# Kernel tuning notes

Measured on AMD Instinct MI355X. Metric: run time of the kernel, lower is better.

The kernel has to match this reference:

```python
import jax, jax.numpy as jnp
import numpy as np

KERNEL_SIZE = 9

def setup_inputs() -> dict:
    key = jax.random.key(0)
    k1, k2 = jax.random.split(key)
    x = jax.random.normal(k1, (32, 16384, 8), dtype=jnp.float32)
    W = jax.random.normal(k2, (8, KERNEL_SIZE), dtype=jnp.float32) * 0.05  # 'random_normal' init
    b = jnp.zeros((1,), dtype=jnp.float32)
    return {"x": x, "W": W, "b": b}

def reference(x, W, b):
    # x: (B, S, F); W: (F, K); b: (1,)
    K = W.shape[1]
    S = x.shape[1]
    new_steps = S - K  # matches original: steps - kernel_size
    base = x[:, :new_steps, :] * W[:, 0]          # (B, N, F)
    peaks = jnp.zeros_like(base)
    # loop over small fixed kernel (K-1 = 8 iterations), vectorized over B, N, F
    for k in range(K - 1):
        shifted = x[:, k:k + new_steps, :] * W[:, k + 1]  # (B, N, F)
        peaks = peaks + jnp.abs(base - shifted)
    return peaks + b  # bias (1,) broadcasts over features, as in original
```

## Files before the change

### kernel.cpp

```cpp
#include <hip/hip_runtime.h>

#define BATCH  32
#define S_DIM  16384
#define F_DIM  8
#define K_DIM  9
#define N_DIM  (S_DIM - K_DIM)
#define NPB    256
#define CHUNKS 528

__global__ __launch_bounds__(256) void peak2peak_kernel(
    const float* __restrict__ x,
    const float* __restrict__ W,
    const float* __restrict__ bias,
    float* __restrict__ out)
{
    __shared__ float4 lds4[CHUNKS];

    const int t  = threadIdx.x;
    const int b  = blockIdx.y;
    const int n0 = blockIdx.x << 8;

    const float* xbase = x + ((long)b * S_DIM + n0) * F_DIM;
    const int climit = 2 * (S_DIM - n0);

#pragma unroll
    for (int i = 0; i < 3; ++i) {
        int c = t + i * 256;
        if (c < CHUNKS && c < climit) {
            float4 v = *reinterpret_cast<const float4*>(xbase + c * 4);
            *reinterpret_cast<float4*>(
                reinterpret_cast<char*>(lds4) + ((c ^ ((c >> 3) & 7)) << 4)) = v;
        }
    }
    __syncthreads();

    const float bb = bias[0];
    float res[F_DIM];

#pragma unroll
    for (int j = 0; j < 2; ++j) {
        float4 rv[8];
#pragma unroll
        for (int k = 0; k < 8; ++k) {
            int row = t + k;
            int byteoff = ((2 * row + j) ^ ((row >> 2) & 7)) << 4;
            rv[k] = *reinterpret_cast<const float4*>(
                reinterpret_cast<const char*>(lds4) + byteoff);
        }
        float rr0[4] = { rv[0].x, rv[0].y, rv[0].z, rv[0].w };
        float basev[4], acc[4];
#pragma unroll
        for (int f = 0; f < 4; ++f) {
            basev[f] = rr0[f] * W[(4 * j + f) * K_DIM];
            acc[f]   = 0.f;
        }
#pragma unroll
        for (int k = 0; k < 8; ++k) {
            float rr[4] = { rv[k].x, rv[k].y, rv[k].z, rv[k].w };
#pragma unroll
            for (int f = 0; f < 4; ++f) {
                acc[f] += fabsf(basev[f] - rr[f] * W[(4 * j + f) * K_DIM + k + 1]);
            }
        }
#pragma unroll
        for (int f = 0; f < 4; ++f) res[4 * j + f] = acc[f] + bb;
    }

    const int n = n0 + t;
    if (n < N_DIM) {
        float* orow = out + ((long)b * N_DIM + n) * F_DIM;
        float4 o0 = { res[0], res[1], res[2], res[3] };
        float4 o1 = { res[4], res[5], res[6], res[7] };
        *reinterpret_cast<float4*>(orow)     = o0;
        *reinterpret_cast<float4*>(orow + 4) = o1;
    }
}

extern "C" void kernel_launch(void* const* d_in, const int* in_sizes, int n_in,
                              void* d_out, int out_size, void* d_ws, size_t ws_size,
                              hipStream_t stream) {
    const float* x    = (const float*)d_in[0];
    const float* W    = (const float*)d_in[1];
    const float* bias = (const float*)d_in[2];
    float* out        = (float*)d_out;

    dim3 grid(S_DIM / NPB, BATCH);
    peak2peak_kernel<<<grid, 256, 0, stream>>>(x, W, bias, out);
}
```

Measured before the change: 12.62 us.

## Replace LDS staging with per-thread register windows computing four outputs each

Removes the shared-memory staging and barrier. Each thread instead loads an 11-row sliding window directly from global memory into registers and computes four consecutive output rows. Outputs are written with nontemporal stores. This trades LDS traffic and synchronisation for redundant, less coalesced global loads that must be served from cache, and for higher register pressure.

```diff
diff --git a/kernel.cpp b/kernel.cpp
--- a/kernel.cpp
+++ b/kernel.cpp
@@ -5,8 +5,9 @@
 #define F_DIM  8
 #define K_DIM  9
 #define N_DIM  (S_DIM - K_DIM)
-#define NPB    256
-#define CHUNKS 528
+#define R_OUT  4
+
+typedef __attribute__((ext_vector_type(4))) float f32x4;
 
 __global__ __launch_bounds__(256) void peak2peak_kernel(
     const float* __restrict__ x,
@@ -14,65 +15,51 @@
     const float* __restrict__ bias,
     float* __restrict__ out)
 {
-    __shared__ float4 lds4[CHUNKS];
+    const int t = threadIdx.x;
+    const int b = blockIdx.y;
+    const int n = (blockIdx.x * 256 + t) * R_OUT;
+    if (n >= N_DIM) return;
 
-    const int t  = threadIdx.x;
-    const int b  = blockIdx.y;
-    const int n0 = blockIdx.x << 8;
+    const float* xrow = x + ((long)b * S_DIM + n) * F_DIM;
 
-    const float* xbase = x + ((long)b * S_DIM + n0) * F_DIM;
-    const int climit = 2 * (S_DIM - n0);
-
+    f32x4 r[R_OUT + 7][2];
 #pragma unroll
-    for (int i = 0; i < 3; ++i) {
-        int c = t + i * 256;
-        if (c < CHUNKS && c < climit) {
-            float4 v = *reinterpret_cast<const float4*>(xbase + c * 4);
-            *reinterpret_cast<float4*>(
-                reinterpret_cast<char*>(lds4) + ((c ^ ((c >> 3) & 7)) << 4)) = v;
-        }
+    for (int i = 0; i < R_OUT + 7; ++i) {
+        r[i][0] = *reinterpret_cast<const f32x4*>(xrow + i * F_DIM);
+        r[i][1] = *reinterpret_cast<const f32x4*>(xrow + i * F_DIM + 4);
     }
-    __syncthreads();
 
     const float bb = bias[0];
-    float res[F_DIM];
 
+    float res[R_OUT][F_DIM];
 #pragma unroll
-    for (int j = 0; j < 2; ++j) {
-        float4 rv[8];
+    for (int i = 0; i < R_OUT; ++i) {
+        float basev[F_DIM], acc[F_DIM];
 #pragma unroll
-        for (int k = 0; k < 8; ++k) {
-            int row = t + k;
-            int byteoff = ((2 * row + j) ^ ((row >> 2) & 7)) << 4;
-            rv[k] = *reinterpret_cast<const float4*>(
-                reinterpret_cast<const char*>(lds4) + byteoff);
-        }
-        float rr0[4] = { rv[0].x, rv[0].y, rv[0].z, rv[0].w };
-        float basev[4], acc[4];
-#pragma unroll
-        for (int f = 0; f < 4; ++f) {
-            basev[f] = rr0[f] * W[(4 * j + f) * K_DIM];
+        for (int f = 0; f < F_DIM; ++f) {
+            basev[f] = r[i][f >> 2][f & 3] * W[f * K_DIM];
             acc[f]   = 0.f;
         }
 #pragma unroll
-        for (int k = 0; k < 8; ++k) {
-            float rr[4] = { rv[k].x, rv[k].y, rv[k].z, rv[k].w };
+        for (int k = 0; k < K_DIM - 1; ++k) {
 #pragma unroll
-            for (int f = 0; f < 4; ++f) {
-                acc[f] += fabsf(basev[f] - rr[f] * W[(4 * j + f) * K_DIM + k + 1]);
+            for (int f = 0; f < F_DIM; ++f) {
+                acc[f] += fabsf(basev[f] - r[i + k][f >> 2][f & 3] * W[f * K_DIM + k + 1]);
             }
         }
 #pragma unroll
-        for (int f = 0; f < 4; ++f) res[4 * j + f] = acc[f] + bb;
+        for (int f = 0; f < F_DIM; ++f) res[i][f] = acc[f] + bb;
     }
 
-    const int n = n0 + t;
-    if (n < N_DIM) {
-        float* orow = out + ((long)b * N_DIM + n) * F_DIM;
-        float4 o0 = { res[0], res[1], res[2], res[3] };
-        float4 o1 = { res[4], res[5], res[6], res[7] };
-        *reinterpret_cast<float4*>(orow)     = o0;
-        *reinterpret_cast<float4*>(orow + 4) = o1;
+    float* orow = out + ((long)b * N_DIM + n) * F_DIM;
+#pragma unroll
+    for (int i = 0; i < R_OUT; ++i) {
+        if (n + i < N_DIM) {
+            f32x4 o0 = { res[i][0], res[i][1], res[i][2], res[i][3] };
+            f32x4 o1 = { res[i][4], res[i][5], res[i][6], res[i][7] };
+            __builtin_nontemporal_store(o0, reinterpret_cast<f32x4*>(orow + i * F_DIM));
+            __builtin_nontemporal_store(o1, reinterpret_cast<f32x4*>(orow + i * F_DIM + 4));
+        }
     }
 }
 
@@ -84,6 +71,9 @@
     const float* bias = (const float*)d_in[2];
     float* out        = (float*)d_out;
 
-    dim3 grid(S_DIM / NPB, BATCH);
+    const int groups_per_batch = (N_DIM + R_OUT - 1) / R_OUT;
+    const int blocks_per_batch = (groups_per_batch + 255) / 256;
+    dim3 grid(blocks_per_batch, BATCH);
+
     peak2peak_kernel<<<grid, 256, 0, stream>>>(x, W, bias, out);
 }
```

After: 37.93 us. 201% more time.

## Compute four outputs per thread with larger tiles to reuse staged rows

Applied to the files above, without the earlier changes.

Each thread now computes four consecutive output rows instead of one, and each block covers 1024 rows instead of 256. A thread reads 12 LDS vectors per feature half where it used to read 8 per single row, so LDS traffic and the halo overhead per output drop. The subtract is folded into an FMA. In exchange the kernel uses more registers and LDS per block and launches fewer blocks (16×32), which lowers occupancy and parallelism for a memory-bound kernel, and the output stores are now strided per thread.

```diff
diff --git a/kernel.cpp b/kernel.cpp
--- a/kernel.cpp
+++ b/kernel.cpp
@@ -5,8 +5,11 @@
 #define F_DIM  8
 #define K_DIM  9
 #define N_DIM  (S_DIM - K_DIM)
-#define NPB    256
-#define CHUNKS 528
+#define NPB    1024
+#define R_OUT  4
+#define CHUNKS 2064
+
+typedef __attribute__((ext_vector_type(4))) float f32x4;
 
 __global__ __launch_bounds__(256) void peak2peak_kernel(
     const float* __restrict__ x,
@@ -14,65 +17,72 @@
     const float* __restrict__ bias,
     float* __restrict__ out)
 {
-    __shared__ float4 lds4[CHUNKS];
+    __shared__ f32x4 lds4[CHUNKS];
 
     const int t  = threadIdx.x;
     const int b  = blockIdx.y;
-    const int n0 = blockIdx.x << 8;
+    const int n0 = blockIdx.x * NPB;
 
     const float* xbase = x + ((long)b * S_DIM + n0) * F_DIM;
     const int climit = 2 * (S_DIM - n0);
 
 #pragma unroll
-    for (int i = 0; i < 3; ++i) {
+    for (int i = 0; i < 9; ++i) {
         int c = t + i * 256;
         if (c < CHUNKS && c < climit) {
-            float4 v = *reinterpret_cast<const float4*>(xbase + c * 4);
-            *reinterpret_cast<float4*>(
+            f32x4 v = *reinterpret_cast<const f32x4*>(xbase + c * 4);
+            *reinterpret_cast<f32x4*>(
                 reinterpret_cast<char*>(lds4) + ((c ^ ((c >> 3) & 7)) << 4)) = v;
         }
     }
     __syncthreads();
 
     const float bb = bias[0];
-    float res[F_DIM];
+    float res[R_OUT][F_DIM];
 
 #pragma unroll
     for (int j = 0; j < 2; ++j) {
-        float4 rv[8];
+        f32x4 rv[R_OUT + 8];
 #pragma unroll
-        for (int k = 0; k < 8; ++k) {
-            int row = t + k;
-            int byteoff = ((2 * row + j) ^ ((row >> 2) & 7)) << 4;
-            rv[k] = *reinterpret_cast<const float4*>(
+        for (int k = 0; k < R_OUT + 8; ++k) {
+            int c = 8 * t + 2 * k + j;
+            int byteoff = (c ^ ((c >> 3) & 7)) << 4;
+            rv[k] = *reinterpret_cast<const f32x4*>(
                 reinterpret_cast<const char*>(lds4) + byteoff);
         }
-        float rr0[4] = { rv[0].x, rv[0].y, rv[0].z, rv[0].w };
-        float basev[4], acc[4];
 #pragma unroll
-        for (int f = 0; f < 4; ++f) {
-            basev[f] = rr0[f] * W[(4 * j + f) * K_DIM];
-            acc[f]   = 0.f;
-        }
-#pragma unroll
-        for (int k = 0; k < 8; ++k) {
-            float rr[4] = { rv[k].x, rv[k].y, rv[k].z, rv[k].w };
+        for (int i = 0; i < R_OUT; ++i) {
+            float basev[4], acc[4];
 #pragma unroll
             for (int f = 0; f < 4; ++f) {
-                acc[f] += fabsf(basev[f] - rr[f] * W[(4 * j + f) * K_DIM + k + 1]);
+                basev[f] = rv[i][f] * W[(4 * j + f) * K_DIM];
+                acc[f]   = 0.f;
             }
+#pragma unroll
+            for (int k = 0; k < 8; ++k) {
+#pragma unroll
+                for (int f = 0; f < 4; ++f) {
+                    float d = __builtin_fmaf(-W[(4 * j + f) * K_DIM + k + 1],
+                                             rv[i + k][f], basev[f]);
+                    acc[f] += fabsf(d);
+                }
+            }
+#pragma unroll
+            for (int f = 0; f < 4; ++f) res[i][4 * j + f] = acc[f] + bb;
         }
-#pragma unroll
-        for (int f = 0; f < 4; ++f) res[4 * j + f] = acc[f] + bb;
     }
 
-    const int n = n0 + t;
-    if (n < N_DIM) {
-        float* orow = out + ((long)b * N_DIM + n) * F_DIM;
-        float4 o0 = { res[0], res[1], res[2], res[3] };
-        float4 o1 = { res[4], res[5], res[6], res[7] };
-        *reinterpret_cast<float4*>(orow)     = o0;
-        *reinterpret_cast<float4*>(orow + 4) = o1;
+    const int nb = n0 + R_OUT * t;
+#pragma unroll
+    for (int i = 0; i < R_OUT; ++i) {
+        int n = nb + i;
+        if (n < N_DIM) {
+            float* orow = out + ((long)b * N_DIM + n) * F_DIM;
+            f32x4 o0 = { res[i][0], res[i][1], res[i][2], res[i][3] };
+            f32x4 o1 = { res[i][4], res[i][5], res[i][6], res[i][7] };
+            *reinterpret_cast<f32x4*>(orow)     = o0;
+            *reinterpret_cast<f32x4*>(orow + 4) = o1;
+        }
     }
 }
 
@@ -84,6 +94,8 @@
     const float* bias = (const float*)d_in[2];
     float* out        = (float*)d_out;
 
-    dim3 grid(S_DIM / NPB, BATCH);
+    const int blocks_per_batch = (N_DIM + NPB - 1) / NPB;
+    dim3 grid(blocks_per_batch, BATCH);
+
     peak2peak_kernel<<<grid, 256, 0, stream>>>(x, W, bias, out);
 }
```

After: 15.34 us. 21.5% more time.
